# Kernel tuning notes

Measured on AMD Instinct MI355X. Metric: run time of the kernel, lower is better.

## Reference

```python
import jax, jax.numpy as jnp
import numpy as np

T, D, E, DE = 50000, 128, 1600000, 3
EPS = 1e-5


def setup_inputs() -> dict:
    key = jax.random.key(0)
    ks = jax.random.split(key, 8)
    H = jax.random.normal(ks[0], (T, D), dtype=jnp.float32)
    edge_index = jax.random.randint(ks[1], (2, E), 0, T, dtype=jnp.int64)
    edge_attr = jax.random.normal(ks[2], (E, DE), dtype=jnp.float32)
    # phi: Linear(D+DE -> D), GELU, Linear(D -> D)
    s1 = 1.0 / np.sqrt(D + DE)
    s2 = 1.0 / np.sqrt(D)
    W1 = jax.random.uniform(ks[3], (D + DE, D), minval=-s1, maxval=s1, dtype=jnp.float32)
    b1 = jax.random.uniform(ks[4], (D,), minval=-s1, maxval=s1, dtype=jnp.float32)
    W2 = jax.random.uniform(ks[5], (D, D), minval=-s2, maxval=s2, dtype=jnp.float32)
    b2 = jax.random.uniform(ks[6], (D,), minval=-s2, maxval=s2, dtype=jnp.float32)
    gamma = jnp.ones((D,), dtype=jnp.float32)
    beta = jnp.zeros((D,), dtype=jnp.float32)
    return {"H": H, "edge_index": edge_index, "edge_attr": edge_attr,
            "W1": W1, "b1": b1, "W2": W2, "b2": b2, "gamma": gamma, "beta": beta}


def reference(H, edge_index, edge_attr, W1, b1, W2, b2, gamma, beta):
    src, dst = edge_index[0], edge_index[1]
    Hj = H[src]                                   # [E, D] gather
    feat = jnp.concatenate([Hj, edge_attr], axis=-1)  # [E, D+DE]
    h = jax.nn.gelu(feat @ W1 + b1, approximate=False)
    m = h @ W2 + b2                               # [E, D] messages
    agg = jax.ops.segment_sum(m, dst, num_segments=H.shape[0])  # scatter-add
    x = H + agg
    mu = jnp.mean(x, axis=-1, keepdims=True)
    var = jnp.mean((x - mu) ** 2, axis=-1, keepdims=True)
    return (x - mu) * jax.lax.rsqrt(var + EPS) * gamma + beta
```

## Files before the change

### kernel.cpp

```cpp
#include <hip/hip_runtime.h>
#include <hip/hip_bf16.h>

typedef unsigned short u16;
typedef unsigned int u32;
typedef __attribute__((ext_vector_type(8))) __bf16 bf16x8;
typedef __attribute__((ext_vector_type(4))) float f32x4;

#define NT 50000
#define NEDGE 1600000
#define GRID 512
#define NWV 8
#define TOTW 4096
#define NBIN 50176

__device__ __forceinline__ u16 f2bf(float f) {
  unsigned x = __float_as_uint(f);
  x += 0x7fffu + ((x >> 16) & 1u);
  return (u16)(x >> 16);
}

__device__ __forceinline__ int swz(int row, int col) {
  return (row << 7) + (col ^ ((row & 7) << 3));
}

__device__ __forceinline__ float gelu(float v) {
  float t = v * (0.797884561f + 0.0356774081f * v * v);
  return v * __builtin_amdgcn_rcpf(1.0f + __expf(-2.0f * t));
}

__device__ __forceinline__ void atomAddF32(float* p, float v) {
#if defined(__has_builtin)
#if __has_builtin(__builtin_amdgcn_global_atomic_fadd_f32)
  __builtin_amdgcn_global_atomic_fadd_f32((__attribute__((address_space(1))) float*)p, v);
  return;
#endif
#endif
  atomicAdd(p, v);
}


__global__ void prep_all(const float* __restrict__ H, u16* __restrict__ Hb,
                         const float* __restrict__ W1, const float* __restrict__ W2,
                         u16* __restrict__ wsw, const float* __restrict__ b1,
                         u16* __restrict__ wx, u32* __restrict__ cnt) {
  int bid = blockIdx.x, tid = threadIdx.x;
  if (bid < 3125) {
    int t = bid * 256 + tid;
    const float4* s = (const float4*)H + (long)t * 2;
    float4 a = s[0], c = s[1];
    int4 pk;
    pk.x = f2bf(a.x) | ((int)f2bf(a.y) << 16);
    pk.y = f2bf(a.z) | ((int)f2bf(a.w) << 16);
    pk.z = f2bf(c.x) | ((int)f2bf(c.y) << 16);
    pk.w = f2bf(c.z) | ((int)f2bf(c.w) << 16);
    ((int4*)Hb)[t] = pk;
  } else if (bid < 3253) {
    int t = (bid - 3125) * 256 + tid;
    int m = t >> 14;
    int p = t & 16383;
    int row = p >> 7;
    int colq = p & 127;
    int k = colq ^ ((row & 7) << 3);
    const float* W = m ? W2 : W1;
    wsw[t] = f2bf(W[k * 128 + row]);
  } else if (bid < 3257) {
    int t = (bid - 3253) * 256 + tid;
    int row = t >> 3, j = t & 7;
    float v = 0.f;
    if (j < 3) v = W1[(128 + j) * 128 + row];
    else if (j == 3) v = b1[row];
    wx[t] = f2bf(v);
  } else if (bid < 3453) {
    int t = (bid - 3257) * 256 + tid;
    if (t < NBIN) cnt[t] = 0;
  } else {
    if (tid < 16) ((int4*)(Hb + (long)NT * 128))[tid] = make_int4(0, 0, 0, 0);
  }
}

__global__ void copy_h(const float4* __restrict__ H, float4* __restrict__ out) {
  int t = blockIdx.x * 256 + threadIdx.x;
  out[t] = H[t];
}


__global__ void hist_g(const int* __restrict__ ei, u32* __restrict__ cnt) {
  int e = blockIdx.x * 256 + threadIdx.x;
  atomicAdd(&cnt[ei[NEDGE + e]], 1u);
}

__global__ void scan_blk(u32* __restrict__ cnt, u32* __restrict__ btot) {
  __shared__ u32 ls[1024];
  int tid = threadIdx.x;
  int bin = blockIdx.x * 1024 + tid;
  u32 c = cnt[bin];
  ls[tid] = c;
  __syncthreads();
  for (int o = 1; o < 1024; o <<= 1) {
    u32 t = (tid >= o) ? ls[tid - o] : 0u;
    __syncthreads();
    ls[tid] += t;
    __syncthreads();
  }
  cnt[bin] = ls[tid] - c;
  if (tid == 1023) btot[blockIdx.x] = ls[1023];
}

__global__ void scan_btot(u32* __restrict__ btot) {
  if (threadIdx.x == 0) {
    u32 run = 0;
    for (int i = 0; i < 49; ++i) { u32 t = btot[i]; btot[i] = run; run += t; }
  }
}

__global__ void fin_base(const u32* __restrict__ cnt, const u32* __restrict__ btot,
                         u32* __restrict__ base, u32* __restrict__ pos) {
  int bin = blockIdx.x * 256 + threadIdx.x;
  if (bin < NT) {
    u32 v = cnt[bin] + btot[bin >> 10];
    base[bin] = v;
    pos[bin] = v;
  }
  if (bin == NT) base[NT] = NEDGE;
}

__global__ void scatter_g(const int* __restrict__ ei, const float* __restrict__ ea,
                          u32* __restrict__ pos, uint2* __restrict__ rec) {
  int e = blockIdx.x * 256 + threadIdx.x;
  int d = ei[NEDGE + e];
  int s = ei[e];
  float e0 = ea[e * 3 + 0], e1 = ea[e * 3 + 1], e2 = ea[e * 3 + 2];
  u32 p = atomicAdd(&pos[d], 1u);
  rec[p] = make_uint2((u32)s | ((u32)f2bf(e0) << 16),
                      (u32)f2bf(e1) | ((u32)f2bf(e2) << 16));
}


__launch_bounds__(512, 2)
__global__ void msg_agg(const u16* __restrict__ Hb,
                        const u16* __restrict__ wsw,
                        const u16* __restrict__ wx,
                        const u32* __restrict__ base,
                        const uint2* __restrict__ rec,
                        u16* __restrict__ hsb) {
  __shared__ __align__(16) u16 lw1[16384];
  __shared__ __align__(16) u16 lw1x[128 * 8];

  const int tid = threadIdx.x;
  {
    const int4* g = (const int4*)wsw;
    int4* d1 = (int4*)lw1;
#pragma unroll
    for (int i = 0; i < 4; ++i) { int c = tid + i * 512; d1[c] = g[c]; }
  }
  if (tid < 128) ((int4*)lw1x)[tid] = ((const int4*)wx)[tid];
  __syncthreads();

  const int wv = tid >> 6, lane = tid & 63;
  const int l15 = lane & 15, l4 = lane >> 4;

  const int gid = blockIdx.x * NWV + wv;
  const int d0 = (int)(((long)gid * NT) / TOTW);
  const int d1i = (int)(((long)(gid + 1) * NT) / TOTW);
  const int nd = d1i - d0;

  for (int b = 0; b < nd; ++b) {
    const int start = (int)base[d0 + b];
    const int cnt = (int)base[d0 + b + 1] - start;

    float racc[8][4];
#pragma unroll
    for (int nt = 0; nt < 8; ++nt)
#pragma unroll
      for (int r = 0; r < 4; ++r) racc[nt][r] = 0.f;

    const int ntile = (cnt + 15) >> 4;
    uint2 r2c = make_uint2(0, 0);
    if (ntile > 0) {
      int i0 = (l15 < cnt) ? l15 : cnt - 1;
      r2c = rec[start + i0];
    }

    for (int t = 0; t < ntile; ++t) {
      int inx = (t + 1) * 16 + l15;
      if (inx >= cnt) inx = cnt - 1;
      uint2 r2n = rec[start + inx];

      const bool valid = (t * 16 + l15) < cnt;
      int src = valid ? (int)(r2c.x & 0xFFFFu) : NT;
      u32 x0 = 0u, x1 = 0u;
      if (l4 == 0 && valid) {
        x0 = (r2c.x >> 16) | (r2c.y << 16);
        x1 = (r2c.y >> 16) | 0x3F800000u;
      }
      int4 xbi = make_int4((int)x0, (int)x1, 0, 0);
      bf16x8 bfrx = *(bf16x8*)&xbi;

      bf16x8 bfc[4];
      {
        const u16* hr = Hb + (long)src * 128;
#pragma unroll
        for (int ks = 0; ks < 4; ++ks)
          bfc[ks] = *(const bf16x8*)(hr + ks * 32 + l4 * 8);
      }

#pragma unroll
      for (int nt = 0; nt < 8; ++nt) {
        bf16x8 afr[4];
#pragma unroll
        for (int ks = 0; ks < 4; ++ks)
          afr[ks] = *(const bf16x8*)&lw1[swz(nt * 16 + l15, ks * 32 + l4 * 8)];
        bf16x8 afrx = *(const bf16x8*)&lw1x[(nt * 16 + l15) * 8];
        f32x4 acc = (f32x4){0.f, 0.f, 0.f, 0.f};
#pragma unroll
        for (int ks = 0; ks < 4; ++ks)
          acc = __builtin_amdgcn_mfma_f32_16x16x32_bf16(bfc[ks], afr[ks], acc, 0, 0, 0);
        acc = __builtin_amdgcn_mfma_f32_16x16x32_bf16(bfrx, afrx, acc, 0, 0, 0);
#pragma unroll
        for (int r = 0; r < 4; ++r)
          racc[nt][r] += gelu(acc[r]);
      }
      r2c = r2n;
    }

    float sv[8];
#pragma unroll
    for (int nt = 0; nt < 8; ++nt) {
      float s = racc[nt][0] + racc[nt][1] + racc[nt][2] + racc[nt][3];
      s += __shfl_xor(s, 16);
      s += __shfl_xor(s, 32);
      sv[nt] = s;
    }
    float sa = (l4 == 0) ? sv[0] : (l4 == 1) ? sv[1] : (l4 == 2) ? sv[2] : sv[3];
    float sb = (l4 == 0) ? sv[4] : (l4 == 1) ? sv[5] : (l4 == 2) ? sv[6] : sv[7];
    u16* hrow = hsb + (long)(d0 + b) * 128;
    hrow[l4 * 16 + l15] = f2bf(sa);
    hrow[64 + l4 * 16 + l15] = f2bf(sb);
  }
}


__launch_bounds__(256)
__global__ void gemm_ln(const u16* __restrict__ hsb,
                        const float* __restrict__ H,
                        const float* __restrict__ b2,
                        const u16* __restrict__ wsw,
                        const u32* __restrict__ base,
                        const float* __restrict__ gamma,
                        const float* __restrict__ beta,
                        float* __restrict__ out) {
  __shared__ __align__(16) u16 lw2[16384];
  const int tid = threadIdx.x;
  {
    const int4* g = (const int4*)wsw + 2048;
    int4* d2 = (int4*)lw2;
#pragma unroll
    for (int i = 0; i < 8; ++i) { int c = tid + i * 256; d2[c] = g[c]; }
  }
  __syncthreads();

  const int wv = tid >> 6, lane = tid & 63;
  const int l15 = lane & 15, l4 = lane >> 4;
  const int r0 = (blockIdx.x * 4 + wv) * 16;

  bf16x8 ha[4];
#pragma unroll
  for (int ks = 0; ks < 4; ++ks)
    ha[ks] = *(const bf16x8*)(hsb + (long)(r0 + l15) * 128 + ks * 32 + l4 * 8);

  float cntr[4];
#pragma unroll
  for (int r = 0; r < 4; ++r) {
    int row = r0 + l4 * 4 + r;
    if (row > NT - 1) row = NT - 1;
    cntr[r] = (float)(base[row + 1] - base[row]);
  }

  float xv[8][4];
#pragma unroll
  for (int nt = 0; nt < 8; ++nt) {
    bf16x8 bfr2[4];
#pragma unroll
    for (int ks = 0; ks < 4; ++ks)
      bfr2[ks] = *(const bf16x8*)&lw2[swz(nt * 16 + l15, ks * 32 + l4 * 8)];
    float b2v = b2[nt * 16 + l15];
    f32x4 acc = (f32x4){0.f, 0.f, 0.f, 0.f};
#pragma unroll
    for (int ks = 0; ks < 4; ++ks)
      acc = __builtin_amdgcn_mfma_f32_16x16x32_bf16(ha[ks], bfr2[ks], acc, 0, 0, 0);
#pragma unroll
    for (int r = 0; r < 4; ++r) {
      int row = r0 + l4 * 4 + r;
      long o = (long)((row < NT) ? row : NT - 1) * 128 + nt * 16 + l15;
      xv[nt][r] = H[o] + acc[r] + cntr[r] * b2v;
    }
  }

  float mu[4], rs[4];
#pragma unroll
  for (int r = 0; r < 4; ++r) {
    float s = 0.f;
#pragma unroll
    for (int nt = 0; nt < 8; ++nt) s += xv[nt][r];
    s += __shfl_xor(s, 1); s += __shfl_xor(s, 2);
    s += __shfl_xor(s, 4); s += __shfl_xor(s, 8);
    mu[r] = s * (1.0f / 128.0f);
    float q = 0.f;
#pragma unroll
    for (int nt = 0; nt < 8; ++nt) {
      float d = xv[nt][r] - mu[r];
      q += d * d;
    }
    q += __shfl_xor(q, 1); q += __shfl_xor(q, 2);
    q += __shfl_xor(q, 4); q += __shfl_xor(q, 8);
    rs[r] = rsqrtf(q * (1.0f / 128.0f) + 1e-5f);
  }

#pragma unroll
  for (int nt = 0; nt < 8; ++nt) {
    int col = nt * 16 + l15;
    float g = gamma[col], bb = beta[col];
#pragma unroll
    for (int r = 0; r < 4; ++r) {
      int row = r0 + l4 * 4 + r;
      if (row < NT)
        out[(long)row * 128 + col] = (xv[nt][r] - mu[r]) * rs[r] * g + bb;
    }
  }
}


template <int BF16H>
__launch_bounds__(256, 1)
__global__ void msg_atomic(const float* __restrict__ H,
                           const u16* __restrict__ Hb,
                           const int* __restrict__ ei,
                           const float* __restrict__ ea,
                           const float* __restrict__ W1,
                           const float* __restrict__ b1,
                           const float* __restrict__ b2,
                           const u16* __restrict__ wsw,
                           float* __restrict__ out) {
  __shared__ __align__(16) u16 lw1[16384];
  __shared__ __align__(16) u16 lw2[16384];
  __shared__ __align__(16) u16 lh[4 * 2048];
  __shared__ __align__(16) float lep[5][128];

  const int tid = threadIdx.x;
  {
    const int4* g = (const int4*)wsw;
    int4* d1 = (int4*)lw1;
    int4* d2 = (int4*)lw2;
#pragma unroll
    for (int i = 0; i < 8; ++i) {
      int c = tid + i * 256;
      d1[c] = g[c];
      d2[c] = g[2048 + c];
    }
  }
  if (tid < 128) {
    lep[0][tid] = b1[tid];
    lep[1][tid] = W1[128 * 128 + tid];
    lep[2][tid] = W1[129 * 128 + tid];
    lep[3][tid] = W1[130 * 128 + tid];
    lep[4][tid] = b2[tid];
  }
  __syncthreads();

  const int wv = tid >> 6, lane = tid & 63;
  const int l15 = lane & 15, l4 = lane >> 4;
  u16* lhw = lh + wv * 2048;
  const int gwid = blockIdx.x * 4 + wv;

  for (int g = gwid; g < NEDGE / 16; g += 4096) {
    const int eb = g * 16;
    int src = ei[eb + l15];
    float ea0 = ea[(eb + l15) * 3 + 0], ea1 = ea[(eb + l15) * 3 + 1], ea2 = ea[(eb + l15) * 3 + 2];

    bf16x8 bfr[4];
    if (BF16H) {
      const u16* hr = Hb + (long)src * 128;
#pragma unroll
      for (int ks = 0; ks < 4; ++ks)
        bfr[ks] = *(const bf16x8*)(hr + ks * 32 + l4 * 8);
    } else {
      const float* hr = H + (long)src * 128;
#pragma unroll
      for (int ks = 0; ks < 4; ++ks) {
        float4 a = *(const float4*)(hr + ks * 32 + l4 * 8);
        float4 c = *(const float4*)(hr + ks * 32 + l4 * 8 + 4);
        int4 pk;
        pk.x = f2bf(a.x) | ((int)f2bf(a.y) << 16);
        pk.y = f2bf(a.z) | ((int)f2bf(a.w) << 16);
        pk.z = f2bf(c.x) | ((int)f2bf(c.y) << 16);
        pk.w = f2bf(c.z) | ((int)f2bf(c.w) << 16);
        bfr[ks] = *(bf16x8*)&pk;
      }
    }

#pragma unroll
    for (int nt = 0; nt < 8; ++nt) {
      bf16x8 afr[4];
#pragma unroll
      for (int ks = 0; ks < 4; ++ks)
        afr[ks] = *(const bf16x8*)&lw1[swz(nt * 16 + l15, ks * 32 + l4 * 8)];
      f32x4 acc = (f32x4){0.f, 0.f, 0.f, 0.f};
#pragma unroll
      for (int ks = 0; ks < 4; ++ks)
        acc = __builtin_amdgcn_mfma_f32_16x16x32_bf16(afr[ks], bfr[ks], acc, 0, 0, 0);
      f32x4 b1v = *(const f32x4*)&lep[0][nt * 16 + l4 * 4];
      f32x4 w0v = *(const f32x4*)&lep[1][nt * 16 + l4 * 4];
      f32x4 w1v = *(const f32x4*)&lep[2][nt * 16 + l4 * 4];
      f32x4 w2v = *(const f32x4*)&lep[3][nt * 16 + l4 * 4];
      float hv[4];
#pragma unroll
      for (int r = 0; r < 4; ++r) {
        float v = acc[r] + b1v[r] + ea0 * w0v[r] + ea1 * w1v[r] + ea2 * w2v[r];
        hv[r] = gelu(v);
      }
      int2 hp;
      hp.x = f2bf(hv[0]) | ((int)f2bf(hv[1]) << 16);
      hp.y = f2bf(hv[2]) | ((int)f2bf(hv[3]) << 16);
      *(int2*)&lhw[swz(l15, nt * 16 + l4 * 4)] = hp;
    }

    asm volatile("" ::: "memory");

    bf16x8 ha[4];
#pragma unroll
    for (int ks = 0; ks < 4; ++ks)
      ha[ks] = *(const bf16x8*)&lhw[swz(l15, ks * 32 + l4 * 8)];
    int drow[4];
#pragma unroll
    for (int r = 0; r < 4; ++r) drow[r] = ei[NEDGE + eb + l4 * 4 + r];

#pragma unroll
    for (int nt = 0; nt < 8; ++nt) {
      bf16x8 bfr2[4];
#pragma unroll
      for (int ks = 0; ks < 4; ++ks)
        bfr2[ks] = *(const bf16x8*)&lw2[swz(nt * 16 + l15, ks * 32 + l4 * 8)];
      float b2v = lep[4][nt * 16 + l15];
      f32x4 acc = (f32x4){0.f, 0.f, 0.f, 0.f};
#pragma unroll
      for (int ks = 0; ks < 4; ++ks)
        acc = __builtin_amdgcn_mfma_f32_16x16x32_bf16(ha[ks], bfr2[ks], acc, 0, 0, 0);
#pragma unroll
      for (int r = 0; r < 4; ++r)
        atomAddF32(out + (long)drow[r] * 128 + nt * 16 + l15, acc[r] + b2v);
    }
  }
}

__global__ void ln_rows(float* __restrict__ out, const float* __restrict__ gamma,
                        const float* __restrict__ beta) {
  int wave = threadIdx.x >> 6, lane = threadIdx.x & 63;
  int row = blockIdx.x * 4 + wave;
  float2 v = *(const float2*)(out + (long)row * 128 + lane * 2);
  float s = v.x + v.y;
#pragma unroll
  for (int off = 32; off; off >>= 1) s += __shfl_xor(s, off);
  float mu = s * (1.0f / 128.0f);
  float dx = v.x - mu, dy = v.y - mu;
  float q = dx * dx + dy * dy;
#pragma unroll
  for (int off = 32; off; off >>= 1) q += __shfl_xor(q, off);
  float rs = rsqrtf(q * (1.0f / 128.0f) + 1e-5f);
  float2 g = *(const float2*)(gamma + lane * 2);
  float2 b = *(const float2*)(beta + lane * 2);
  float2 o;
  o.x = dx * rs * g.x + b.x;
  o.y = dy * rs * g.y + b.y;
  *(float2*)(out + (long)row * 128 + lane * 2) = o;
}

extern "C" void kernel_launch(void* const* d_in, const int* in_sizes, int n_in,
                              void* d_out, int out_size, void* d_ws, size_t ws_size,
                              hipStream_t stream) {
  const float* H   = (const float*)d_in[0];
  const int* ei    = (const int*)d_in[1];
  const float* ea  = (const float*)d_in[2];
  const float* W1  = (const float*)d_in[3];
  const float* b1  = (const float*)d_in[4];
  const float* W2  = (const float*)d_in[5];
  const float* b2  = (const float*)d_in[6];
  const float* gam = (const float*)d_in[7];
  const float* bet = (const float*)d_in[8];
  float* out = (float*)d_out;

  char* ws = (char*)d_ws;
  u16* wsw   = (u16*)ws;
  u16* wx    = (u16*)(ws + 65536);
  u16* Hb    = (u16*)(ws + 67584);
  u32* cnt   = (u32*)(ws + 12867840);
  u32* base  = (u32*)(ws + 13068544);
  u32* pos   = (u32*)(ws + 13268560);
  u32* btot  = (u32*)(ws + 13468560);
  uint2* rec = (uint2*)(ws + 13468816);
  u16* hsb   = (u16*)(ws + 26268816);
  const size_t NEED_FULL = 39081104;
  const size_t NEED_HB = 12867840;

  if (ws_size >= NEED_FULL) {
    prep_all<<<3454, 256, 0, stream>>>(H, Hb, W1, W2, wsw, b1, wx, cnt);
    hist_g<<<6250, 256, 0, stream>>>(ei, cnt);
    scan_blk<<<49, 1024, 0, stream>>>(cnt, btot);
    scan_btot<<<1, 64, 0, stream>>>(btot);
    fin_base<<<196, 256, 0, stream>>>(cnt, btot, base, pos);
    scatter_g<<<6250, 256, 0, stream>>>(ei, ea, pos, rec);
    msg_agg<<<GRID, 512, 0, stream>>>(Hb, wsw, wx, base, rec, hsb);
    gemm_ln<<<782, 256, 0, stream>>>(hsb, H, b2, wsw, base, gam, bet, out);
  } else if (ws_size >= NEED_HB) {
    prep_all<<<3454, 256, 0, stream>>>(H, Hb, W1, W2, wsw, b1, wx, cnt);
    copy_h<<<6250, 256, 0, stream>>>((const float4*)H, (float4*)out);
    msg_atomic<1><<<1024, 256, 0, stream>>>(H, Hb, ei, ea, W1, b1, b2, wsw, out);
    ln_rows<<<12500, 256, 0, stream>>>(out, gam, bet);
  } else {
    copy_h<<<6250, 256, 0, stream>>>((const float4*)H, (float4*)out);
    msg_atomic<0><<<1024, 256, 0, stream>>>(H, Hb, ei, ea, W1, b1, b2, wsw, out);
    ln_rows<<<12500, 256, 0, stream>>>(out, gam, bet);
  }
}
```

Measured before the change: 359.5 us.

## Keep W1 fragments in registers and fuse scan passes via last-block pattern

The message kernel now loads each wave's W1 MFMA fragments straight from global memory into registers once, instead of staging W1 in LDS and re-reading it for every edge tile. Blocks shrink to 256 threads and the grid doubles. Separately, the block-total scan and the base/pos finalisation are folded into scan_blk: the last block to finish, detected with an atomic counter, does that work, which removes two kernel launches. The risks are higher register pressure (128 extra VGPRs per lane), which can cut occupancy, and a serial tail in the single finishing block.

```diff
diff --git a/kernel.cpp b/kernel.cpp
--- a/kernel.cpp
+++ b/kernel.cpp
@@ -8,8 +8,8 @@
 
 #define NT 50000
 #define NEDGE 1600000
-#define GRID 512
-#define NWV 8
+#define GRID 1024
+#define NWV 4
 #define TOTW 4096
 #define NBIN 50176
 
@@ -42,7 +42,8 @@
 __global__ void prep_all(const float* __restrict__ H, u16* __restrict__ Hb,
                          const float* __restrict__ W1, const float* __restrict__ W2,
                          u16* __restrict__ wsw, const float* __restrict__ b1,
-                         u16* __restrict__ wx, u32* __restrict__ cnt) {
+                         u16* __restrict__ wx, u32* __restrict__ cnt,
+                         u32* __restrict__ done) {
   int bid = blockIdx.x, tid = threadIdx.x;
   if (bid < 3125) {
     int t = bid * 256 + tid;
@@ -75,6 +76,7 @@
     if (t < NBIN) cnt[t] = 0;
   } else {
     if (tid < 16) ((int4*)(Hb + (long)NT * 128))[tid] = make_int4(0, 0, 0, 0);
+    if (tid == 32) done[0] = 0u;
   }
 }
 
@@ -89,8 +91,12 @@
   atomicAdd(&cnt[ei[NEDGE + e]], 1u);
 }
 
-__global__ void scan_blk(u32* __restrict__ cnt, u32* __restrict__ btot) {
+__global__ void scan_blk(u32* __restrict__ cnt, u32* __restrict__ btot,
+                         u32* __restrict__ base, u32* __restrict__ pos,
+                         u32* __restrict__ done) {
   __shared__ u32 ls[1024];
+  __shared__ u32 bt[64];
+  __shared__ int lastBlk;
   int tid = threadIdx.x;
   int bin = blockIdx.x * 1024 + tid;
   u32 c = cnt[bin];
@@ -104,24 +110,28 @@
   }
   cnt[bin] = ls[tid] - c;
   if (tid == 1023) btot[blockIdx.x] = ls[1023];
-}
-
-__global__ void scan_btot(u32* __restrict__ btot) {
-  if (threadIdx.x == 0) {
+  __threadfence();
+  __syncthreads();
+  if (tid == 0) lastBlk = (atomicAdd(done, 1u) == 48u) ? 1 : 0;
+  __syncthreads();
+  if (!lastBlk) return;
+
+  if (tid < 49) bt[tid] = atomicAdd(&btot[tid], 0u);
+  __syncthreads();
+  if (tid == 0) {
     u32 run = 0;
-    for (int i = 0; i < 49; ++i) { u32 t = btot[i]; btot[i] = run; run += t; }
-  }
-}
-
-__global__ void fin_base(const u32* __restrict__ cnt, const u32* __restrict__ btot,
-                         u32* __restrict__ base, u32* __restrict__ pos) {
-  int bin = blockIdx.x * 256 + threadIdx.x;
-  if (bin < NT) {
-    u32 v = cnt[bin] + btot[bin >> 10];
-    base[bin] = v;
-    pos[bin] = v;
-  }
-  if (bin == NT) base[NT] = NEDGE;
+    for (int i = 0; i < 49; ++i) { u32 t = bt[i]; bt[i] = run; run += t; }
+  }
+  __syncthreads();
+  for (int b = tid; b <= NT; b += 1024) {
+    if (b < NT) {
+      u32 v = atomicAdd(&cnt[b], 0u) + bt[b >> 10];
+      base[b] = v;
+      pos[b] = v;
+    } else {
+      base[NT] = NEDGE;
+    }
+  }
 }
 
 __global__ void scatter_g(const int* __restrict__ ei, const float* __restrict__ ea,
@@ -136,28 +146,28 @@
 }
 
 
-__launch_bounds__(512, 2)
+__launch_bounds__(256)
 __global__ void msg_agg(const u16* __restrict__ Hb,
                         const u16* __restrict__ wsw,
                         const u16* __restrict__ wx,
                         const u32* __restrict__ base,
                         const uint2* __restrict__ rec,
                         u16* __restrict__ hsb) {
-  __shared__ __align__(16) u16 lw1[16384];
   __shared__ __align__(16) u16 lw1x[128 * 8];
 
   const int tid = threadIdx.x;
-  {
-    const int4* g = (const int4*)wsw;
-    int4* d1 = (int4*)lw1;
-#pragma unroll
-    for (int i = 0; i < 4; ++i) { int c = tid + i * 512; d1[c] = g[c]; }
-  }
   if (tid < 128) ((int4*)lw1x)[tid] = ((const int4*)wx)[tid];
   __syncthreads();
 
   const int wv = tid >> 6, lane = tid & 63;
   const int l15 = lane & 15, l4 = lane >> 4;
+
+  bf16x8 af[8][4];
+#pragma unroll
+  for (int nt = 0; nt < 8; ++nt)
+#pragma unroll
+    for (int ks = 0; ks < 4; ++ks)
+      af[nt][ks] = *(const bf16x8*)&wsw[swz(nt * 16 + l15, ks * 32 + l4 * 8)];
 
   const int gid = blockIdx.x * NWV + wv;
   const int d0 = (int)(((long)gid * NT) / TOTW);
@@ -206,15 +216,11 @@
 
 #pragma unroll
       for (int nt = 0; nt < 8; ++nt) {
-        bf16x8 afr[4];
-#pragma unroll
-        for (int ks = 0; ks < 4; ++ks)
-          afr[ks] = *(const bf16x8*)&lw1[swz(nt * 16 + l15, ks * 32 + l4 * 8)];
         bf16x8 afrx = *(const bf16x8*)&lw1x[(nt * 16 + l15) * 8];
         f32x4 acc = (f32x4){0.f, 0.f, 0.f, 0.f};
 #pragma unroll
         for (int ks = 0; ks < 4; ++ks)
-          acc = __builtin_amdgcn_mfma_f32_16x16x32_bf16(bfc[ks], afr[ks], acc, 0, 0, 0);
+          acc = __builtin_amdgcn_mfma_f32_16x16x32_bf16(bfc[ks], af[nt][ks], acc, 0, 0, 0);
         acc = __builtin_amdgcn_mfma_f32_16x16x32_bf16(bfrx, afrx, acc, 0, 0, 0);
 #pragma unroll
         for (int r = 0; r < 4; ++r)
@@ -496,22 +502,21 @@
   u32* base  = (u32*)(ws + 13068544);
   u32* pos   = (u32*)(ws + 13268560);
   u32* btot  = (u32*)(ws + 13468560);
-  uint2* rec = (uint2*)(ws + 13468816);
-  u16* hsb   = (u16*)(ws + 26268816);
-  const size_t NEED_FULL = 39081104;
+  u32* done  = (u32*)(ws + 13468816);
+  uint2* rec = (uint2*)(ws + 13468832);
+  u16* hsb   = (u16*)(ws + 26268832);
+  const size_t NEED_FULL = 39081120;
   const size_t NEED_HB = 12867840;
 
   if (ws_size >= NEED_FULL) {
-    prep_all<<<3454, 256, 0, stream>>>(H, Hb, W1, W2, wsw, b1, wx, cnt);
+    prep_all<<<3454, 256, 0, stream>>>(H, Hb, W1, W2, wsw, b1, wx, cnt, done);
     hist_g<<<6250, 256, 0, stream>>>(ei, cnt);
-    scan_blk<<<49, 1024, 0, stream>>>(cnt, btot);
-    scan_btot<<<1, 64, 0, stream>>>(btot);
-    fin_base<<<196, 256, 0, stream>>>(cnt, btot, base, pos);
+    scan_blk<<<49, 1024, 0, stream>>>(cnt, btot, base, pos, done);
     scatter_g<<<6250, 256, 0, stream>>>(ei, ea, pos, rec);
-    msg_agg<<<GRID, 512, 0, stream>>>(Hb, wsw, wx, base, rec, hsb);
+    msg_agg<<<GRID, 256, 0, stream>>>(Hb, wsw, wx, base, rec, hsb);
     gemm_ln<<<782, 256, 0, stream>>>(hsb, H, b2, wsw, base, gam, bet, out);
   } else if (ws_size >= NEED_HB) {
-    prep_all<<<3454, 256, 0, stream>>>(H, Hb, W1, W2, wsw, b1, wx, cnt);
+    prep_all<<<3454, 256, 0, stream>>>(H, Hb, W1, W2, wsw, b1, wx, cnt, done);
     copy_h<<<6250, 256, 0, stream>>>((const float4*)H, (float4*)out);
     msg_atomic<1><<<1024, 256, 0, stream>>>(H, Hb, ei, ea, W1, b1, b2, wsw, out);
     ln_rows<<<12500, 256, 0, stream>>>(out, gam, bet);
```

New measurement: 385.5 us. +7.2%, slower.

## Split msg_agg output columns across wave pairs with W1 held in registers

Applied to the files above, without the earlier changes.

Each destination segment is now handled by two waves, each covering half of the 128 hidden columns. Each wave keeps its 64-column slice of W1 in registers instead of reading it from shared memory on every edge tile. The aim is to remove LDS traffic and the large shared allocation, at the cost of gathering each source row of H twice and doing the edge-record loop twice. GELU is also rewritten to use exp2 with folded constants, and the launch becomes 2048 blocks of 256 threads.

```diff
diff --git a/kernel.cpp b/kernel.cpp
--- a/kernel.cpp
+++ b/kernel.cpp
@@ -8,9 +8,8 @@
 
 #define NT 50000
 #define NEDGE 1600000
-#define GRID 512
-#define NWV 8
-#define TOTW 4096
+#define GRID2 2048
+#define NPAIR 4096
 #define NBIN 50176
 
 __device__ __forceinline__ u16 f2bf(float f) {
@@ -24,8 +23,10 @@
 }
 
 __device__ __forceinline__ float gelu(float v) {
-  float t = v * (0.797884561f + 0.0356774081f * v * v);
-  return v * __builtin_amdgcn_rcpf(1.0f + __expf(-2.0f * t));
+  float u = v * v;
+  float arg = v * __builtin_fmaf(-0.1029434f, u, -2.3022082f);
+  float e = __builtin_amdgcn_exp2f(arg);
+  return v * __builtin_amdgcn_rcpf(1.0f + e);
 }
 
 __device__ __forceinline__ void atomAddF32(float* p, float v) {
@@ -136,41 +137,44 @@
 }
 
 
-__launch_bounds__(512, 2)
+__launch_bounds__(256)
 __global__ void msg_agg(const u16* __restrict__ Hb,
                         const u16* __restrict__ wsw,
                         const u16* __restrict__ wx,
                         const u32* __restrict__ base,
                         const uint2* __restrict__ rec,
                         u16* __restrict__ hsb) {
-  __shared__ __align__(16) u16 lw1[16384];
   __shared__ __align__(16) u16 lw1x[128 * 8];
 
   const int tid = threadIdx.x;
-  {
-    const int4* g = (const int4*)wsw;
-    int4* d1 = (int4*)lw1;
-#pragma unroll
-    for (int i = 0; i < 4; ++i) { int c = tid + i * 512; d1[c] = g[c]; }
-  }
   if (tid < 128) ((int4*)lw1x)[tid] = ((const int4*)wx)[tid];
   __syncthreads();
 
   const int wv = tid >> 6, lane = tid & 63;
   const int l15 = lane & 15, l4 = lane >> 4;
 
-  const int gid = blockIdx.x * NWV + wv;
-  const int d0 = (int)(((long)gid * NT) / TOTW);
-  const int d1i = (int)(((long)(gid + 1) * NT) / TOTW);
+  const int gid = blockIdx.x * 4 + wv;
+  const int pair = gid >> 1;
+  const int nh = gid & 1;
+
+  bf16x8 af[4][4];
+#pragma unroll
+  for (int nt = 0; nt < 4; ++nt)
+#pragma unroll
+    for (int ks = 0; ks < 4; ++ks)
+      af[nt][ks] = *(const bf16x8*)&wsw[swz((nh * 4 + nt) * 16 + l15, ks * 32 + l4 * 8)];
+
+  const int d0 = (int)(((long)pair * NT) / NPAIR);
+  const int d1i = (int)(((long)(pair + 1) * NT) / NPAIR);
   const int nd = d1i - d0;
 
   for (int b = 0; b < nd; ++b) {
     const int start = (int)base[d0 + b];
     const int cnt = (int)base[d0 + b + 1] - start;
 
-    float racc[8][4];
-#pragma unroll
-    for (int nt = 0; nt < 8; ++nt)
+    float racc[4][4];
+#pragma unroll
+    for (int nt = 0; nt < 4; ++nt)
 #pragma unroll
       for (int r = 0; r < 4; ++r) racc[nt][r] = 0.f;
 
@@ -205,16 +209,12 @@
       }
 
 #pragma unroll
-      for (int nt = 0; nt < 8; ++nt) {
-        bf16x8 afr[4];
+      for (int nt = 0; nt < 4; ++nt) {
+        bf16x8 afrx = *(const bf16x8*)&lw1x[((nh * 4 + nt) * 16 + l15) * 8];
+        f32x4 acc = (f32x4){0.f, 0.f, 0.f, 0.f};
 #pragma unroll
         for (int ks = 0; ks < 4; ++ks)
-          afr[ks] = *(const bf16x8*)&lw1[swz(nt * 16 + l15, ks * 32 + l4 * 8)];
-        bf16x8 afrx = *(const bf16x8*)&lw1x[(nt * 16 + l15) * 8];
-        f32x4 acc = (f32x4){0.f, 0.f, 0.f, 0.f};
-#pragma unroll
-        for (int ks = 0; ks < 4; ++ks)
-          acc = __builtin_amdgcn_mfma_f32_16x16x32_bf16(bfc[ks], afr[ks], acc, 0, 0, 0);
+          acc = __builtin_amdgcn_mfma_f32_16x16x32_bf16(bfc[ks], af[nt][ks], acc, 0, 0, 0);
         acc = __builtin_amdgcn_mfma_f32_16x16x32_bf16(bfrx, afrx, acc, 0, 0, 0);
 #pragma unroll
         for (int r = 0; r < 4; ++r)
@@ -223,19 +223,17 @@
       r2c = r2n;
     }
 
-    float sv[8];
-#pragma unroll
-    for (int nt = 0; nt < 8; ++nt) {
+    float sv[4];
+#pragma unroll
+    for (int nt = 0; nt < 4; ++nt) {
       float s = racc[nt][0] + racc[nt][1] + racc[nt][2] + racc[nt][3];
       s += __shfl_xor(s, 16);
       s += __shfl_xor(s, 32);
       sv[nt] = s;
     }
     float sa = (l4 == 0) ? sv[0] : (l4 == 1) ? sv[1] : (l4 == 2) ? sv[2] : sv[3];
-    float sb = (l4 == 0) ? sv[4] : (l4 == 1) ? sv[5] : (l4 == 2) ? sv[6] : sv[7];
     u16* hrow = hsb + (long)(d0 + b) * 128;
-    hrow[l4 * 16 + l15] = f2bf(sa);
-    hrow[64 + l4 * 16 + l15] = f2bf(sb);
+    hrow[nh * 64 + l4 * 16 + l15] = f2bf(sa);
   }
 }
 
@@ -496,9 +494,9 @@
   u32* base  = (u32*)(ws + 13068544);
   u32* pos   = (u32*)(ws + 13268560);
   u32* btot  = (u32*)(ws + 13468560);
-  uint2* rec = (uint2*)(ws + 13468816);
-  u16* hsb   = (u16*)(ws + 26268816);
-  const size_t NEED_FULL = 39081104;
+  uint2* rec = (uint2*)(ws + 13468832);
+  u16* hsb   = (u16*)(ws + 26268832);
+  const size_t NEED_FULL = 39081120;
   const size_t NEED_HB = 12867840;
 
   if (ws_size >= NEED_FULL) {
@@ -508,7 +506,7 @@
     scan_btot<<<1, 64, 0, stream>>>(btot);
     fin_base<<<196, 256, 0, stream>>>(cnt, btot, base, pos);
     scatter_g<<<6250, 256, 0, stream>>>(ei, ea, pos, rec);
-    msg_agg<<<GRID, 512, 0, stream>>>(Hb, wsw, wx, base, rec, hsb);
+    msg_agg<<<GRID2, 256, 0, stream>>>(Hb, wsw, wx, base, rec, hsb);
     gemm_ln<<<782, 256, 0, stream>>>(hsb, H, b2, wsw, base, gam, bet, out);
   } else if (ws_size >= NEED_HB) {
     prep_all<<<3454, 256, 0, stream>>>(H, Hb, W1, W2, wsw, b1, wx, cnt);
```

Measured after the change: 372.8 us. +3.7%, slower.
